# Kernel tuning notes

Hardware: AMD Instinct MI355X
Metric: run time of the kernel (lower is better)

## Reference

```python
import jax, jax.numpy as jnp
import numpy as np
from jax import lax

RANK = 8
ALPHA = 16.0
SCALING = ALPHA / RANK  # 2.0
C_IN, C_OUT, KH, KW = 128, 256, 3, 3


def setup_inputs() -> dict:
    key = jax.random.key(0)
    k1, k2, k3, k4, k5 = jax.random.split(key, 5)
    x = jax.random.normal(k1, (16, C_IN, 64, 64), dtype=jnp.float32)
    W = jax.random.normal(k2, (C_OUT, C_IN, KH, KW), dtype=jnp.float32) * 0.05
    b = jax.random.normal(k3, (C_OUT,), dtype=jnp.float32) * 0.05
    lora_A = jax.random.normal(k4, (RANK, C_IN * KH * KW), dtype=jnp.float32) * 0.02
    lora_B = jax.random.normal(k5, (C_OUT, RANK), dtype=jnp.float32) * 0.02
    return {"x": x, "W": W, "b": b, "lora_A": lora_A, "lora_B": lora_B}


def _conv(x, w, stride=(1, 1), padding=((1, 1), (1, 1))):
    return lax.conv_general_dilated(
        x, w, window_strides=stride, padding=padding,
        dimension_numbers=("NCHW", "OIHW", "NCHW"))


def reference(x, W, b, lora_A, lora_B):
    # Base (frozen) conv: [B, C_out, H, W]
    base_out = _conv(x, W) + b[None, :, None, None]
    # LoRA path. The torch code does im2col -> (BL, C_in*kh*kw) @ A.T @ B.T.
    # Because unfold flattens patches channel-major as (C_in, kh, kw), the
    # identical math is: rank-r conv with A reshaped as [rank, C_in, kh, kw],
    # then a 1x1 mix with B. Same result, no im2col materialization.
    A_k = lora_A.reshape(RANK, C_IN, KH, KW)
    h = _conv(x, A_k)                                   # [B, rank, H, W]
    lora_out = jnp.einsum("brhw,or->bohw", h, lora_B) * SCALING
    return base_out + lora_out
```

## Files before the change

kernel.cpp:

```cpp
#include <hip/hip_runtime.h>
#include <hip/hip_bf16.h>


#define CIN   128
#define COUT  256
#define NBAT  16
#define HPAD  66
#define WPAD  66

typedef __bf16 bf16x8 __attribute__((ext_vector_type(8)));
typedef float f32x4 __attribute__((ext_vector_type(4)));

#define XPAD_ELEMS ((size_t)NBAT * HPAD * WPAD * CIN)
#define XPAD_BYTES (XPAD_ELEMS * 2)
#define WT_ELEMS   ((size_t)9 * COUT * CIN)
#define WS_NEED    (XPAD_BYTES + WT_ELEMS * 2)

typedef __attribute__((address_space(1))) void gvoid;
typedef __attribute__((address_space(3))) void lvoid;

__device__ __forceinline__ void load_lds16(const void* g, void* l) {
    __builtin_amdgcn_global_load_lds((gvoid*)g, (lvoid*)l, 16, 0, 0);
}

__global__ void prep_w(const float* __restrict__ W, const float* __restrict__ lA,
                       const float* __restrict__ lB, __hip_bfloat16* __restrict__ Wt) {
    int idx = blockIdx.x * 256 + threadIdx.x;
    int c   = idx & 127;
    int o   = (idx >> 7) & 255;
    int tap = idx >> 15;
    float acc = W[(o * 128 + c) * 9 + tap];
    float s = 0.f;
#pragma unroll
    for (int r = 0; r < 8; ++r)
        s += lB[o * 8 + r] * lA[r * 1152 + c * 9 + tap];
    acc += 2.0f * s;
    Wt[idx] = __float2bfloat16(acc);
}

__global__ void pad_x(const float* __restrict__ x, __bf16* __restrict__ xpad) {
    __shared__ float tile[128][66];
    const int n = blockIdx.x >> 6;
    const int h = blockIdx.x & 63;
    const int t = threadIdx.x;
    const float* src = x + (size_t)n * 128 * 4096 + (size_t)h * 64;
#pragma unroll
    for (int i = 0; i < 8; ++i) {
        int g  = i * 256 + t;
        int c  = g >> 4;
        int w4 = (g & 15) * 4;
        const float4 v = *reinterpret_cast<const float4*>(src + (size_t)c * 4096 + w4);
        tile[c][w4 + 0] = v.x; tile[c][w4 + 1] = v.y;
        tile[c][w4 + 2] = v.z; tile[c][w4 + 3] = v.w;
    }
    __syncthreads();
    __bf16* dst = xpad + ((size_t)(n * 66 + h + 1) * 66 + 1) * 128;
#pragma unroll
    for (int i = 0; i < 4; ++i) {
        int g  = i * 256 + t;
        int w  = g >> 4;
        int c0 = (g & 15) * 8;
        bf16x8 v;
#pragma unroll
        for (int j = 0; j < 8; ++j) v[j] = (__bf16)tile[c0 + j][w];
        *reinterpret_cast<bf16x8*>(dst + (size_t)w * 128 + c0) = v;
    }
    bf16x8 z = {};
    __bf16* rowbase = xpad + (size_t)(n * 66 + h + 1) * 66 * 128;
    if (t < 32) {
        int ww = (t < 16) ? 0 : 65;
        int c0 = (t & 15) * 8;
        *reinterpret_cast<bf16x8*>(rowbase + (size_t)ww * 128 + c0) = z;
    }
    if (h == 0 || h == 63) {
        __bf16* hrow = xpad + (size_t)(n * 66 + (h == 0 ? 0 : 65)) * 66 * 128;
        for (int i = t; i < 66 * 16; i += 256)
            *reinterpret_cast<bf16x8*>(hrow + (size_t)i * 8) = z;
    }
}

__global__ void __launch_bounds__(256) conv_mfma(
    const __bf16* __restrict__ xpad, const __bf16* __restrict__ Wt,
    const float* __restrict__ bias, float* __restrict__ out) {
    __shared__ __align__(16) __bf16 As[128 * 64];
    __shared__ __align__(16) __bf16 Bs[128 * 64];

    const int tid  = threadIdx.x;
    const int wv   = tid >> 6;
    const int lane = tid & 63;

    const int pt    = blockIdx.x;
    const int ob    = blockIdx.y;
    const int n     = pt >> 5;
    const int h0    = (pt & 31) << 1;
    const int obase = ob << 7;

    const int swz = ((lane >> 3) << 7) + ((((lane & 7) ^ (lane >> 3)) & 7) << 3);

    const __bf16* aG[4];
    const __bf16* bG[4];
#pragma unroll
    for (int j = 0; j < 4; ++j) {
        const int row0 = wv * 32 + j * 8;
        aG[j] = Wt + (obase + row0) * 128 + swz;
        const int p0 = row0;
        bG[j] = xpad + (((size_t)(n * 66 + h0 + (p0 >> 6)) * 66 + (p0 & 63)) * 128) + swz;
    }

    const int wo = (wv >> 1) << 6;
    const int wp = (wv & 1) << 6;

    int arow[4], brow[4], qo[2];
#pragma unroll
    for (int i = 0; i < 4; ++i) {
        arow[i] = (wo + i * 16 + (lane & 15)) << 6;
        brow[i] = (wp + i * 16 + (lane & 15)) << 6;
    }
#pragma unroll
    for (int s = 0; s < 2; ++s)
        qo[s] = ((((lane >> 4) + s * 4) ^ (lane & 7)) << 3);

    f32x4 acc[4][4] = {};

#pragma unroll
    for (int tap = 0; tap < 9; ++tap) {
        const int kh = tap / 3, kw = tap % 3;
        const int aoff_t = tap * (COUT * CIN);
        const int boff_t = (kh * 66 + kw) * 128;
#pragma unroll
        for (int cb = 0; cb < 2; ++cb) {
            const int ao = aoff_t + cb * 64;
            const int bo = boff_t + cb * 64;
            __syncthreads();
#pragma unroll
            for (int j = 0; j < 4; ++j) {
                load_lds16(aG[j] + ao, &As[wv * 2048 + j * 512]);
                load_lds16(bG[j] + bo, &Bs[wv * 2048 + j * 512]);
            }
            __syncthreads();
#pragma unroll
            for (int s = 0; s < 2; ++s) {
                bf16x8 af[4], bfr[4];
#pragma unroll
                for (int i = 0; i < 4; ++i) {
                    af[i]  = *reinterpret_cast<const bf16x8*>(&As[arow[i] + qo[s]]);
                    bfr[i] = *reinterpret_cast<const bf16x8*>(&Bs[brow[i] + qo[s]]);
                }
#pragma unroll
                for (int mi = 0; mi < 4; ++mi)
#pragma unroll
                    for (int ni = 0; ni < 4; ++ni)
                        acc[mi][ni] = __builtin_amdgcn_mfma_f32_16x16x32_bf16(
                            af[mi], bfr[ni], acc[mi][ni], 0, 0, 0);
            }
        }
    }

    const int col  = lane & 15;
    const int orow = (lane >> 4) << 2;
    const int h    = h0 + (wv & 1);
#pragma unroll
    for (int mi = 0; mi < 4; ++mi) {
        const int obm = obase + wo + mi * 16 + orow;
#pragma unroll
        for (int j = 0; j < 4; ++j) {
            const int o = obm + j;
            const float bj = bias[o];
            float* orow_ptr = out + (((size_t)n * 256 + o) * 64 + h) * 64;
#pragma unroll
            for (int ni = 0; ni < 4; ++ni)
                orow_ptr[ni * 16 + col] = acc[mi][ni][j] + bj;
        }
    }
}

__global__ void conv_naive(const float* __restrict__ x, const float* __restrict__ W,
                           const float* __restrict__ b, const float* __restrict__ lA,
                           const float* __restrict__ lB, float* __restrict__ out) {
    int idx = blockIdx.x * 256 + threadIdx.x;
    int w = idx & 63, h = (idx >> 6) & 63, o = (idx >> 12) & 255, n = idx >> 20;
    float acc = b[o];
    float hr[8] = {0, 0, 0, 0, 0, 0, 0, 0};
    for (int c = 0; c < 128; ++c)
        for (int kh = 0; kh < 3; ++kh) {
            int hy = h + kh - 1;
            if (hy < 0 || hy > 63) continue;
            for (int kw = 0; kw < 3; ++kw) {
                int wx = w + kw - 1;
                if (wx < 0 || wx > 63) continue;
                float xv = x[((n * 128 + c) * 64 + hy) * 64 + wx];
                int ka = c * 9 + kh * 3 + kw;
                acc += W[(o * 128 + c) * 9 + kh * 3 + kw] * xv;
#pragma unroll
                for (int r = 0; r < 8; ++r) hr[r] += lA[r * 1152 + ka] * xv;
            }
        }
    float ls = 0.f;
#pragma unroll
    for (int r = 0; r < 8; ++r) ls += lB[o * 8 + r] * hr[r];
    out[idx] = acc + 2.0f * ls;
}

extern "C" void kernel_launch(void* const* d_in, const int* in_sizes, int n_in,
                              void* d_out, int out_size, void* d_ws, size_t ws_size,
                              hipStream_t stream) {
    const float* x  = (const float*)d_in[0];
    const float* W  = (const float*)d_in[1];
    const float* b  = (const float*)d_in[2];
    const float* lA = (const float*)d_in[3];
    const float* lB = (const float*)d_in[4];
    float* out = (float*)d_out;

    if (ws_size < WS_NEED) {
        conv_naive<<<out_size / 256, 256, 0, stream>>>(x, W, b, lA, lB, out);
        return;
    }

    __bf16* xpad = (__bf16*)d_ws;
    __hip_bfloat16* Wt = (__hip_bfloat16*)((char*)d_ws + XPAD_BYTES);

    pad_x<<<NBAT * 64, 256, 0, stream>>>(x, xpad);
    prep_w<<<(int)(WT_ELEMS / 256), 256, 0, stream>>>(W, lA, lB, Wt);
    conv_mfma<<<dim3(512, 2), 256, 0, stream>>>(xpad, (const __bf16*)Wt, b, out);
}
```

Before: 143.4 us.

## Fuse prep kernels, swizzle pad tile, double-buffer larger conv tile

Merges the input padding and weight-folding kernels into one launch, with the weight blocks computing all nine taps per thread. It XOR-swizzles the transpose tile in LDS to cut bank conflicts. The conv kernel now uses 512-thread blocks covering all 256 output channels and four rows, with a double-buffered 128KB LDS pipeline that prefetches the next K-slice during the MFMAs, plus setprio hints. The larger tile improves reuse and removes one barrier per step, but yields only 256 blocks and heavy LDS and register use, which may limit occupancy.

```diff
diff --git a/kernel.cpp b/kernel.cpp
--- a/kernel.cpp
+++ b/kernel.cpp
@@ -23,26 +23,33 @@
     __builtin_amdgcn_global_load_lds((gvoid*)g, (lvoid*)l, 16, 0, 0);
 }
 
-__global__ void prep_w(const float* __restrict__ W, const float* __restrict__ lA,
-                       const float* __restrict__ lB, __hip_bfloat16* __restrict__ Wt) {
-    int idx = blockIdx.x * 256 + threadIdx.x;
-    int c   = idx & 127;
-    int o   = (idx >> 7) & 255;
-    int tap = idx >> 15;
-    float acc = W[(o * 128 + c) * 9 + tap];
-    float s = 0.f;
-#pragma unroll
-    for (int r = 0; r < 8; ++r)
-        s += lB[o * 8 + r] * lA[r * 1152 + c * 9 + tap];
-    acc += 2.0f * s;
-    Wt[idx] = __float2bfloat16(acc);
-}
-
-__global__ void pad_x(const float* __restrict__ x, __bf16* __restrict__ xpad) {
+__global__ void pad_prep(const float* __restrict__ x, __bf16* __restrict__ xpad,
+                         const float* __restrict__ W, const float* __restrict__ lA,
+                         const float* __restrict__ lB, __hip_bfloat16* __restrict__ Wt) {
     __shared__ float tile[128][66];
+    const int t = threadIdx.x;
+
+    if (blockIdx.x >= 1024) {
+        const int idx = (blockIdx.x - 1024) * 256 + t;
+        const int c = idx & 127;
+        const int o = idx >> 7;
+        float lb[8];
+#pragma unroll
+        for (int r = 0; r < 8; ++r) lb[r] = lB[o * 8 + r];
+#pragma unroll
+        for (int tap = 0; tap < 9; ++tap) {
+            float acc = W[(o * 128 + c) * 9 + tap];
+            float s = 0.f;
+#pragma unroll
+            for (int r = 0; r < 8; ++r)
+                s += lb[r] * lA[r * 1152 + c * 9 + tap];
+            Wt[tap * 32768 + idx] = __float2bfloat16(acc + 2.0f * s);
+        }
+        return;
+    }
+
     const int n = blockIdx.x >> 6;
     const int h = blockIdx.x & 63;
-    const int t = threadIdx.x;
     const float* src = x + (size_t)n * 128 * 4096 + (size_t)h * 64;
 #pragma unroll
     for (int i = 0; i < 8; ++i) {
@@ -50,8 +57,9 @@
         int c  = g >> 4;
         int w4 = (g & 15) * 4;
         const float4 v = *reinterpret_cast<const float4*>(src + (size_t)c * 4096 + w4);
-        tile[c][w4 + 0] = v.x; tile[c][w4 + 1] = v.y;
-        tile[c][w4 + 2] = v.z; tile[c][w4 + 3] = v.w;
+        const int wb = w4 ^ (((c >> 3) & 7) << 2);
+        tile[c][wb + 0] = v.x; tile[c][wb + 1] = v.y;
+        tile[c][wb + 2] = v.z; tile[c][wb + 3] = v.w;
     }
     __syncthreads();
     __bf16* dst = xpad + ((size_t)(n * 66 + h + 1) * 66 + 1) * 128;
@@ -60,9 +68,10 @@
         int g  = i * 256 + t;
         int w  = g >> 4;
         int c0 = (g & 15) * 8;
+        const int swr = ((c0 >> 3) & 7) << 2;
         bf16x8 v;
 #pragma unroll
-        for (int j = 0; j < 8; ++j) v[j] = (__bf16)tile[c0 + j][w];
+        for (int j = 0; j < 8; ++j) v[j] = (__bf16)tile[c0 + j][w ^ swr];
         *reinterpret_cast<bf16x8*>(dst + (size_t)w * 128 + c0) = v;
     }
     bf16x8 z = {};
@@ -79,21 +88,17 @@
     }
 }
 
-__global__ void __launch_bounds__(256) conv_mfma(
+__global__ void __launch_bounds__(512, 2) conv_mfma(
     const __bf16* __restrict__ xpad, const __bf16* __restrict__ Wt,
     const float* __restrict__ bias, float* __restrict__ out) {
-    __shared__ __align__(16) __bf16 As[128 * 64];
-    __shared__ __align__(16) __bf16 Bs[128 * 64];
+    __shared__ __align__(16) __bf16 lds[65536];
 
     const int tid  = threadIdx.x;
     const int wv   = tid >> 6;
     const int lane = tid & 63;
 
-    const int pt    = blockIdx.x;
-    const int ob    = blockIdx.y;
-    const int n     = pt >> 5;
-    const int h0    = (pt & 31) << 1;
-    const int obase = ob << 7;
+    const int n  = blockIdx.x >> 4;
+    const int h0 = (blockIdx.x & 15) << 2;
 
     const int swz = ((lane >> 3) << 7) + ((((lane & 7) ^ (lane >> 3)) & 7) << 3);
 
@@ -101,67 +106,76 @@
     const __bf16* bG[4];
 #pragma unroll
     for (int j = 0; j < 4; ++j) {
-        const int row0 = wv * 32 + j * 8;
-        aG[j] = Wt + (obase + row0) * 128 + swz;
-        const int p0 = row0;
-        bG[j] = xpad + (((size_t)(n * 66 + h0 + (p0 >> 6)) * 66 + (p0 & 63)) * 128) + swz;
-    }
-
-    const int wo = (wv >> 1) << 6;
-    const int wp = (wv & 1) << 6;
-
-    int arow[4], brow[4], qo[2];
-#pragma unroll
-    for (int i = 0; i < 4; ++i) {
-        arow[i] = (wo + i * 16 + (lane & 15)) << 6;
-        brow[i] = (wp + i * 16 + (lane & 15)) << 6;
-    }
+        const int r0 = wv * 32 + j * 8;
+        aG[j] = Wt + (size_t)r0 * 128 + swz;
+        bG[j] = xpad + (((size_t)(n * 66 + h0 + (r0 >> 6)) * 66 + (r0 & 63)) * 128) + swz;
+    }
+
+    const int wo   = (wv >> 2) << 7;
+    const int wpix = (wv & 3) << 6;
+    const int a_rd = (wo + (lane & 15)) << 6;
+    const int b_rd = (wpix + (lane & 15)) << 6;
+    int qo[2];
 #pragma unroll
     for (int s = 0; s < 2; ++s)
-        qo[s] = ((((lane >> 4) + s * 4) ^ (lane & 7)) << 3);
-
-    f32x4 acc[4][4] = {};
-
-#pragma unroll
-    for (int tap = 0; tap < 9; ++tap) {
-        const int kh = tap / 3, kw = tap % 3;
-        const int aoff_t = tap * (COUT * CIN);
-        const int boff_t = (kh * 66 + kw) * 128;
-#pragma unroll
-        for (int cb = 0; cb < 2; ++cb) {
-            const int ao = aoff_t + cb * 64;
-            const int bo = boff_t + cb * 64;
-            __syncthreads();
+        qo[s] = ((((lane >> 4) + s * 4) ^ (lane & 7)) & 7) << 3;
+
+    f32x4 acc[8][4] = {};
+
+#pragma unroll
+    for (int j = 0; j < 4; ++j) {
+        load_lds16(aG[j], lds + (wv * 32 + j * 8) * 64);
+        load_lds16(bG[j], lds + 32768 + (wv * 32 + j * 8) * 64);
+    }
+
+#pragma unroll
+    for (int t = 0; t < 18; ++t) {
+        asm volatile("s_waitcnt vmcnt(0) lgkmcnt(0)" ::: "memory");
+        __builtin_amdgcn_sched_barrier(0);
+        __builtin_amdgcn_s_barrier();
+
+        if (t + 1 < 18) {
+            const int t1   = t + 1;
+            const int tap1 = t1 >> 1, cb1 = t1 & 1;
+            const int ao = tap1 * 32768 + cb1 * 64;
+            const int bo = ((tap1 / 3) * 66 + (tap1 % 3)) * 128 + cb1 * 64;
+            __bf16* Ad = lds + (t1 & 1) * 16384;
+            __bf16* Bd = lds + 32768 + (t1 & 1) * 16384;
 #pragma unroll
             for (int j = 0; j < 4; ++j) {
-                load_lds16(aG[j] + ao, &As[wv * 2048 + j * 512]);
-                load_lds16(bG[j] + bo, &Bs[wv * 2048 + j * 512]);
+                load_lds16(aG[j] + ao, Ad + (wv * 32 + j * 8) * 64);
+                load_lds16(bG[j] + bo, Bd + (wv * 32 + j * 8) * 64);
             }
-            __syncthreads();
-#pragma unroll
-            for (int s = 0; s < 2; ++s) {
-                bf16x8 af[4], bfr[4];
-#pragma unroll
-                for (int i = 0; i < 4; ++i) {
-                    af[i]  = *reinterpret_cast<const bf16x8*>(&As[arow[i] + qo[s]]);
-                    bfr[i] = *reinterpret_cast<const bf16x8*>(&Bs[brow[i] + qo[s]]);
-                }
-#pragma unroll
-                for (int mi = 0; mi < 4; ++mi)
-#pragma unroll
-                    for (int ni = 0; ni < 4; ++ni)
-                        acc[mi][ni] = __builtin_amdgcn_mfma_f32_16x16x32_bf16(
-                            af[mi], bfr[ni], acc[mi][ni], 0, 0, 0);
-            }
+        }
+
+        const __bf16* Ab = lds + (t & 1) * 16384 + a_rd;
+        const __bf16* Bb = lds + 32768 + (t & 1) * 16384 + b_rd;
+#pragma unroll
+        for (int s = 0; s < 2; ++s) {
+            bf16x8 af[8], bfr[4];
+#pragma unroll
+            for (int ni = 0; ni < 4; ++ni)
+                bfr[ni] = *reinterpret_cast<const bf16x8*>(Bb + (ni << 10) + qo[s]);
+#pragma unroll
+            for (int mi = 0; mi < 8; ++mi)
+                af[mi] = *reinterpret_cast<const bf16x8*>(Ab + (mi << 10) + qo[s]);
+            __builtin_amdgcn_s_setprio(1);
+#pragma unroll
+            for (int mi = 0; mi < 8; ++mi)
+#pragma unroll
+                for (int ni = 0; ni < 4; ++ni)
+                    acc[mi][ni] = __builtin_amdgcn_mfma_f32_16x16x32_bf16(
+                        af[mi], bfr[ni], acc[mi][ni], 0, 0, 0);
+            __builtin_amdgcn_s_setprio(0);
         }
     }
 
     const int col  = lane & 15;
     const int orow = (lane >> 4) << 2;
-    const int h    = h0 + (wv & 1);
-#pragma unroll
-    for (int mi = 0; mi < 4; ++mi) {
-        const int obm = obase + wo + mi * 16 + orow;
+    const int h    = h0 + (wpix >> 6);
+#pragma unroll
+    for (int mi = 0; mi < 8; ++mi) {
+        const int obm = wo + mi * 16 + orow;
 #pragma unroll
         for (int j = 0; j < 4; ++j) {
             const int o = obm + j;
@@ -219,7 +233,6 @@
     __bf16* xpad = (__bf16*)d_ws;
     __hip_bfloat16* Wt = (__hip_bfloat16*)((char*)d_ws + XPAD_BYTES);
 
-    pad_x<<<NBAT * 64, 256, 0, stream>>>(x, xpad);
-    prep_w<<<(int)(WT_ELEMS / 256), 256, 0, stream>>>(W, lA, lB, Wt);
-    conv_mfma<<<dim3(512, 2), 256, 0, stream>>>(xpad, (const __bf16*)Wt, b, out);
-}
+    pad_prep<<<1024 + 128, 256, 0, stream>>>(x, xpad, W, lA, lB, Wt);
+    conv_mfma<<<256, 512, 0, stream>>>(xpad, (const __bf16*)Wt, b, out);
+}
```

Result: faster. 129.1 us (-10.0%).
